# Optimization experiments

Hardware: AMD Instinct MI355X
Metric: run time of the kernel (lower is better)

## Reference

```python
import jax, jax.numpy as jnp
import numpy as np

NUM_CELLS = 2048
CELL_DIM = 256
N_STATES = 131072


def setup_inputs() -> dict:
    key = jax.random.key(0)
    k1, k2 = jax.random.split(key)
    x = jax.random.normal(k1, (N_STATES, CELL_DIM), dtype=jnp.float32)
    placeCells = jax.random.normal(k2, (NUM_CELLS, CELL_DIM), dtype=jnp.float32)
    return {"x": x, "placeCells": placeCells}


def reference(x, placeCells):
    # states: (N, cellDim); sims: (N, numCells); output: (N,) int argmax
    states = x.reshape(-1, CELL_DIM)
    sims = jnp.matmul(states, placeCells.T)  # (N, numCells) dense similarity
    return jnp.argmax(sims, axis=1)
```

## Files before the change

kernel.cpp:

```cpp
#include <hip/hip_runtime.h>
#include <float.h>
#include <stdint.h>

#define NUM_CELLS 2048
#define CELL_DIM  256
#define N_STATES  131072

typedef _Float16 half8 __attribute__((ext_vector_type(8)));
typedef float    f32x4 __attribute__((ext_vector_type(4)));

#define M1 0.10f
#define M2 0.004f
#define CAP1 32768
#define CAP2 4096

#define WS_C1 0
#define WS_C2 4
#define WS_L1 1024
#define WS_L2 (1024 + 4 * CAP1)
#define WS_PH 262144
#define WS_PL (262144 + 1048576)
#define WS_NEEDED (WS_PL + 1048576)

__device__ __forceinline__ void gld_lds16(const void* g, void* l) {
    __builtin_amdgcn_global_load_lds(
        (const __attribute__((address_space(1))) void*)g,
        (__attribute__((address_space(3))) void*)l, 16, 0, 0);
}

__global__ void prep_p(const float* __restrict__ p, _Float16* __restrict__ ph,
                       _Float16* __restrict__ pl, int* __restrict__ c1,
                       int* __restrict__ c2) {
    int d = blockIdx.x * 256 + threadIdx.x;
    if (d == 0) { *c1 = 0; *c2 = 0; }
    int l = d & 63, kf = (d >> 6) & 7, ct = d >> 9;
    int cell = ct * 16 + (l & 15);
    int k0 = kf * 32 + (l >> 4) * 8;
    const float* s = p + cell * 256 + k0;
    float4 a = *(const float4*)s, b = *(const float4*)(s + 4);
    float v[8] = {a.x, a.y, a.z, a.w, b.x, b.y, b.z, b.w};
    half8 h, lo;
#pragma unroll
    for (int j = 0; j < 8; ++j) {
        _Float16 hi = (_Float16)v[j];
        h[j] = hi;
        lo[j] = (_Float16)((v[j] - (float)hi) * 2048.0f);
    }
    *(half8*)(ph + (size_t)d * 8) = h;
    *(half8*)(pl + (size_t)d * 8) = lo;
}

__launch_bounds__(512, 2)
__global__ void pc_gemm1(const float* __restrict__ x, const _Float16* __restrict__ ph,
                         int* __restrict__ out, int* __restrict__ c1,
                         int* __restrict__ l1) {
    __shared__ _Float16 smem[32768];

    const int tid = threadIdx.x;
    const int l = tid & 63;
    const int w = tid >> 6;
    const int wr = w >> 2, wc = w & 3;

    const float* xg = x + (size_t)blockIdx.x * (128 * CELL_DIM);
#pragma unroll
    for (int i = 0; i < 8; ++i) {
        int d = tid + i * 512;
        int dl = d & 63, kf = (d >> 6) & 7, rt = d >> 9;
        int row = rt * 16 + (dl & 15);
        int k0 = kf * 32 + (dl >> 4) * 8;
        const float* s = xg + row * 256 + k0;
        float4 a = *(const float4*)s, b = *(const float4*)(s + 4);
        half8 h;
        h[0] = (_Float16)a.x; h[1] = (_Float16)a.y;
        h[2] = (_Float16)a.z; h[3] = (_Float16)a.w;
        h[4] = (_Float16)b.x; h[5] = (_Float16)b.y;
        h[6] = (_Float16)b.z; h[7] = (_Float16)b.w;
        *(half8*)(smem + d * 8) = h;
    }
    __syncthreads();

    half8 A[4][8];
#pragma unroll
    for (int rt = 0; rt < 4; ++rt)
#pragma unroll
        for (int kf = 0; kf < 8; ++kf)
            A[rt][kf] = *(const half8*)(smem + (((wr * 4 + rt) * 8 + kf) * 64 + l) * 8);
    __syncthreads();

    const char* pbase = (const char*)ph;
    auto stage = [&](int c) {
        char* dst = (char*)smem + (c & 1) * 32768;
        const char* src = pbase + (size_t)c * 32768;
#pragma unroll
        for (int i = 0; i < 4; ++i) {
            int off = w * 4096 + i * 1024;
            gld_lds16(src + off + l * 16, dst + off);
        }
    };

    float t1[16], t2[16];
    int ic[16];
#pragma unroll
    for (int s = 0; s < 16; ++s) { t1[s] = -FLT_MAX; t2[s] = -FLT_MAX; ic[s] = 0; }

    stage(0);
    __syncthreads();

    for (int c = 0; c < 32; ++c) {
        if (c < 31) stage(c + 1);
        const _Float16* pb = smem + (c & 1) * 16384 + wc * 4096;
        f32x4 a0 = {}, a1 = {}, a2 = {}, a3 = {};
#pragma unroll
        for (int kf = 0; kf < 8; ++kf) {
            half8 B = *(const half8*)(pb + kf * 512 + l * 8);
            a0 = __builtin_amdgcn_mfma_f32_16x16x32_f16(A[0][kf], B, a0, 0, 0, 0);
            a1 = __builtin_amdgcn_mfma_f32_16x16x32_f16(A[1][kf], B, a1, 0, 0, 0);
            a2 = __builtin_amdgcn_mfma_f32_16x16x32_f16(A[2][kf], B, a2, 0, 0, 0);
            a3 = __builtin_amdgcn_mfma_f32_16x16x32_f16(A[3][kf], B, a3, 0, 0, 0);
        }
#define UPD(ACC, RT)                                                       \
        _Pragma("unroll")                                                  \
        for (int reg = 0; reg < 4; ++reg) {                                \
            int s = (RT) * 4 + reg;                                        \
            float v = (ACC)[reg];                                          \
            float nt2 = __builtin_amdgcn_fmed3f(t1[s], t2[s], v);          \
            ic[s] = (v > t1[s]) ? c : ic[s];                               \
            t1[s] = fmaxf(t1[s], v);                                       \
            t2[s] = nt2;                                                   \
        }
        UPD(a0, 0) UPD(a1, 1) UPD(a2, 2) UPD(a3, 3)
#undef UPD
        __syncthreads();
    }

    int idx[16];
#pragma unroll
    for (int s = 0; s < 16; ++s) idx[s] = ic[s] * 64 + wc * 16 + (l & 15);
#pragma unroll
    for (int m = 1; m <= 8; m <<= 1) {
#pragma unroll
        for (int s = 0; s < 16; ++s) {
            float ot1 = __shfl_xor(t1[s], m, 64);
            int   oi  = __shfl_xor(idx[s], m, 64);
            float ot2 = __shfl_xor(t2[s], m, 64);
            float nt2 = fmaxf(fminf(t1[s], ot1), fmaxf(t2[s], ot2));
            if (ot1 > t1[s] || (ot1 == t1[s] && oi < idx[s])) { t1[s] = ot1; idx[s] = oi; }
            t2[s] = nt2;
        }
    }

    float* rT1 = (float*)smem;
    int*   rI1 = (int*)smem + 512;
    float* rT2 = (float*)smem + 1024;
    if ((l & 15) == 0) {
#pragma unroll
        for (int rt = 0; rt < 4; ++rt)
#pragma unroll
            for (int reg = 0; reg < 4; ++reg) {
                int s = rt * 4 + reg;
                int row = wr * 64 + rt * 16 + (l >> 4) * 4 + reg;
                rT1[row * 4 + wc] = t1[s];
                rI1[row * 4 + wc] = idx[s];
                rT2[row * 4 + wc] = t2[s];
            }
    }
    __syncthreads();
    if (tid < 128) {
        float T1 = -FLT_MAX, T2 = -FLT_MAX; int I1 = 0x7FFFFFFF;
#pragma unroll
        for (int g = 0; g < 4; ++g) {
            float v1 = rT1[tid * 4 + g];
            int   vi = rI1[tid * 4 + g];
            float v2 = rT2[tid * 4 + g];
            float nt2 = fmaxf(fminf(T1, v1), fmaxf(T2, v2));
            if (v1 > T1 || (v1 == T1 && vi < I1)) { T1 = v1; I1 = vi; }
            T2 = nt2;
        }
        int grow = blockIdx.x * 128 + tid;
        out[grow] = I1;
        if (T1 - T2 < M1) {
            int pos = atomicAdd(c1, 1);
            if (pos < CAP1) l1[pos] = grow;
        }
    }
}

__launch_bounds__(256, 2)
__global__ void pc_rescue2(const float* __restrict__ x, const _Float16* __restrict__ ph,
                           const _Float16* __restrict__ pl,
                           const int* __restrict__ c1, const int* __restrict__ l1,
                           int* __restrict__ out, int* __restrict__ c2,
                           int* __restrict__ l2) {
    __shared__ _Float16 sB[32768];
    const int n = *c1;
    const int base = blockIdx.x * 32;
    if (base >= n) return;
    const int tid = threadIdx.x;
    const int l = tid & 63, w = tid >> 6;
    const int wr = w >> 1, wc = w & 1;

    const int rslot = base + wr * 16 + (l & 15);
    const int my_row = l1[rslot < n ? rslot : (n - 1)];

    half8 Ah[8], Al[8];
#pragma unroll
    for (int kf = 0; kf < 8; ++kf) {
        const float* s = x + (size_t)my_row * 256 + kf * 32 + (l >> 4) * 8;
        float4 a = *(const float4*)s, b = *(const float4*)(s + 4);
        float v[8] = {a.x, a.y, a.z, a.w, b.x, b.y, b.z, b.w};
#pragma unroll
        for (int j = 0; j < 8; ++j) {
            _Float16 hi = (_Float16)v[j];
            Ah[kf][j] = hi;
            Al[kf][j] = (_Float16)((v[j] - (float)hi) * 2048.0f);
        }
    }

    auto stageB = [&](int c) {
        char* dst = (char*)sB + (c & 1) * 32768;
        const char* sh = (const char*)ph + (size_t)c * 16384;
        const char* sl = (const char*)pl + (size_t)c * 16384;
#pragma unroll
        for (int i = 0; i < 4; ++i) {
            int off = w * 4096 + i * 1024;
            gld_lds16(sh + off + l * 16, dst + off);
            gld_lds16(sl + off + l * 16, dst + 16384 + off);
        }
    };

    float t1[4], t2[4];
    int ic[4];
#pragma unroll
    for (int s = 0; s < 4; ++s) { t1[s] = -FLT_MAX; t2[s] = -FLT_MAX; ic[s] = 0; }

    stageB(0);
    __syncthreads();
    for (int c = 0; c < 64; ++c) {
        if (c < 63) stageB(c + 1);
        const _Float16* bh = sB + (c & 1) * 16384 + wc * 4096;
        const _Float16* bl = bh + 8192;
        f32x4 hh = {}, hl = {}, lh = {};
#pragma unroll
        for (int kf = 0; kf < 8; ++kf) {
            half8 Bh = *(const half8*)(bh + kf * 512 + l * 8);
            half8 Bl = *(const half8*)(bl + kf * 512 + l * 8);
            hh = __builtin_amdgcn_mfma_f32_16x16x32_f16(Ah[kf], Bh, hh, 0, 0, 0);
            hl = __builtin_amdgcn_mfma_f32_16x16x32_f16(Ah[kf], Bl, hl, 0, 0, 0);
            lh = __builtin_amdgcn_mfma_f32_16x16x32_f16(Al[kf], Bh, lh, 0, 0, 0);
        }
#pragma unroll
        for (int reg = 0; reg < 4; ++reg) {
            float v = hh[reg] + (hl[reg] + lh[reg]) * (1.0f / 2048.0f);
            float nt2 = __builtin_amdgcn_fmed3f(t1[reg], t2[reg], v);
            ic[reg] = (v > t1[reg]) ? c : ic[reg];
            t1[reg] = fmaxf(t1[reg], v);
            t2[reg] = nt2;
        }
        __syncthreads();
    }

    int idx[4];
#pragma unroll
    for (int s = 0; s < 4; ++s) idx[s] = ic[s] * 32 + wc * 16 + (l & 15);
#pragma unroll
    for (int m = 1; m <= 8; m <<= 1) {
#pragma unroll
        for (int s = 0; s < 4; ++s) {
            float ot1 = __shfl_xor(t1[s], m, 64);
            int   oi  = __shfl_xor(idx[s], m, 64);
            float ot2 = __shfl_xor(t2[s], m, 64);
            float nt2 = fmaxf(fminf(t1[s], ot1), fmaxf(t2[s], ot2));
            if (ot1 > t1[s] || (ot1 == t1[s] && oi < idx[s])) { t1[s] = ot1; idx[s] = oi; }
            t2[s] = nt2;
        }
    }

    float* rT1 = (float*)sB;
    int*   rI1 = (int*)sB + 64;
    float* rT2 = (float*)sB + 128;
    if ((l & 15) == 0) {
#pragma unroll
        for (int reg = 0; reg < 4; ++reg) {
            int row = wr * 16 + (l >> 4) * 4 + reg;
            rT1[row * 2 + wc] = t1[reg];
            rI1[row * 2 + wc] = idx[reg];
            rT2[row * 2 + wc] = t2[reg];
        }
    }
    __syncthreads();
    if (tid < 32) {
        float T1 = -FLT_MAX, T2 = -FLT_MAX; int I1 = 0x7FFFFFFF;
#pragma unroll
        for (int g = 0; g < 2; ++g) {
            float v1 = rT1[tid * 2 + g];
            int   vi = rI1[tid * 2 + g];
            float v2 = rT2[tid * 2 + g];
            float nt2 = fmaxf(fminf(T1, v1), fmaxf(T2, v2));
            if (v1 > T1 || (v1 == T1 && vi < I1)) { T1 = v1; I1 = vi; }
            T2 = nt2;
        }
        int slot = base + tid;
        if (slot < n) {
            int grow = l1[slot];
            out[grow] = I1;
            if (T1 - T2 < M2) {
                int pos = atomicAdd(c2, 1);
                if (pos < CAP2) l2[pos] = grow;
            }
        }
    }
}

__global__ void rescue3(const float* __restrict__ x, const float* __restrict__ p,
                        const int* __restrict__ count, const int* __restrict__ list,
                        int* __restrict__ out) {
    __shared__ float xrow[256];
    __shared__ float pch[32][260];
    __shared__ float red2[32][9];
    __shared__ float bvs[32];
    __shared__ int   bis[32];
    const int tid = threadIdx.x;
    const int n = *count;
    for (int e = blockIdx.x; e < n; e += gridDim.x) {
        const int row = list[e];
        __syncthreads();
        if (tid < 64) {
            float4 v = *(const float4*)(x + (size_t)row * 256 + tid * 4);
            *(float4*)(&xrow[tid * 4]) = v;
        }
        float bv = -FLT_MAX; int bi = 0;
        const int cell = tid & 31, kq = tid >> 5;
        for (int c0 = 0; c0 < NUM_CELLS; c0 += 32) {
            __syncthreads();
#pragma unroll
            for (int i = 0; i < 8; ++i) {
                int f = tid + i * 256;
                int cr = f >> 6, k4 = (f & 63) * 4;
                float4 v = *(const float4*)(p + (size_t)(c0 + cr) * 256 + k4);
                *(float4*)(&pch[cr][k4]) = v;
            }
            __syncthreads();
            float s = 0.f;
#pragma unroll
            for (int j = 0; j < 8; ++j) {
                float4 pv = *(const float4*)(&pch[cell][kq * 32 + j * 4]);
                float4 xv = *(const float4*)(&xrow[kq * 32 + j * 4]);
                s = fmaf(xv.x, pv.x, s); s = fmaf(xv.y, pv.y, s);
                s = fmaf(xv.z, pv.z, s); s = fmaf(xv.w, pv.w, s);
            }
            red2[cell][kq] = s;
            __syncthreads();
            if (tid < 32) {
                float dot = 0.f;
#pragma unroll
                for (int q = 0; q < 8; ++q) dot += red2[tid][q];
                if (dot > bv) { bv = dot; bi = c0 + tid; }
            }
        }
        if (tid < 32) { bvs[tid] = bv; bis[tid] = bi; }
        __syncthreads();
        if (tid == 0) {
            float B = bvs[0]; int BI = bis[0];
#pragma unroll
            for (int t = 1; t < 32; ++t)
                if (bvs[t] > B || (bvs[t] == B && bis[t] < BI)) { B = bvs[t]; BI = bis[t]; }
            out[row] = BI;
        }
    }
}

#define BM 64
#define BN 64
#define BK 32
#define XP 260
#define PP 68
__launch_bounds__(256, 2)
__global__ void placecells_argmax_fp32(const float* __restrict__ x,
                                       const float* __restrict__ pc,
                                       int* __restrict__ out) {
    __shared__ float xs[BM * XP];
    __shared__ float ps[BK * PP];
    const int tid = threadIdx.x;
    const int tx = tid & 15;
    const int ty = tid >> 4;
    const float* xg = x + (size_t)blockIdx.x * (BM * CELL_DIM);
#pragma unroll
    for (int i = 0; i < 16; ++i) {
        int f = tid + i * 256;
        int s = f >> 6, k4 = (f & 63) << 2;
        *(float4*)(&xs[s * XP + k4]) = *(const float4*)(xg + s * CELL_DIM + k4);
    }
    __syncthreads();
    float runv[4]; int runi[4];
#pragma unroll
    for (int si = 0; si < 4; ++si) { runv[si] = -FLT_MAX; runi[si] = 0; }
    for (int jc = 0; jc < NUM_CELLS; jc += BN) {
        float acc[4][4];
#pragma unroll
        for (int si = 0; si < 4; ++si)
#pragma unroll
            for (int cj = 0; cj < 4; ++cj) acc[si][cj] = 0.0f;
        for (int kc = 0; kc < CELL_DIM; kc += BK) {
            __syncthreads();
#pragma unroll
            for (int i = 0; i < 2; ++i) {
                int f = tid + i * 256;
                int c = f >> 3, k4 = (f & 7) << 2;
                float4 v = *(const float4*)(pc + (size_t)(jc + c) * CELL_DIM + kc + k4);
                ps[(k4 + 0) * PP + c] = v.x; ps[(k4 + 1) * PP + c] = v.y;
                ps[(k4 + 2) * PP + c] = v.z; ps[(k4 + 3) * PP + c] = v.w;
            }
            __syncthreads();
#pragma unroll
            for (int kk = 0; kk < BK; kk += 4) {
                float4 xv[4];
#pragma unroll
                for (int si = 0; si < 4; ++si)
                    xv[si] = *(const float4*)(&xs[(ty * 4 + si) * XP + kc + kk]);
#pragma unroll
                for (int kt = 0; kt < 4; ++kt) {
                    float4 pv = *(const float4*)(&ps[(kk + kt) * PP + tx * 4]);
#pragma unroll
                    for (int si = 0; si < 4; ++si) {
                        float xk = (kt == 0) ? xv[si].x : (kt == 1) ? xv[si].y :
                                   (kt == 2) ? xv[si].z : xv[si].w;
                        acc[si][0] = fmaf(xk, pv.x, acc[si][0]);
                        acc[si][1] = fmaf(xk, pv.y, acc[si][1]);
                        acc[si][2] = fmaf(xk, pv.z, acc[si][2]);
                        acc[si][3] = fmaf(xk, pv.w, acc[si][3]);
                    }
                }
            }
        }
#pragma unroll
        for (int si = 0; si < 4; ++si)
#pragma unroll
            for (int cj = 0; cj < 4; ++cj) {
                int idx = jc + tx * 4 + cj;
                if (acc[si][cj] > runv[si]) { runv[si] = acc[si][cj]; runi[si] = idx; }
            }
    }
    __syncthreads();
    float* rv = ps; int* ri = (int*)(ps + 1024);
#pragma unroll
    for (int si = 0; si < 4; ++si) {
        int s = ty * 4 + si;
        rv[s * 16 + tx] = runv[si]; ri[s * 16 + tx] = runi[si];
    }
    __syncthreads();
    if (tid < BM) {
        float bv = rv[tid * 16]; int bi = ri[tid * 16];
#pragma unroll
        for (int t = 1; t < 16; ++t) {
            float v = rv[tid * 16 + t]; int i = ri[tid * 16 + t];
            if (v > bv || (v == bv && i < bi)) { bv = v; bi = i; }
        }
        out[(size_t)blockIdx.x * BM + tid] = bi;
    }
}

extern "C" void kernel_launch(void* const* d_in, const int* in_sizes, int n_in,
                              void* d_out, int out_size, void* d_ws, size_t ws_size,
                              hipStream_t stream) {
    const float* x  = (const float*)d_in[0];
    const float* pc = (const float*)d_in[1];
    int* out = (int*)d_out;

    if (ws_size >= (size_t)WS_NEEDED) {
        char* ws = (char*)d_ws;
        int* c1 = (int*)(ws + WS_C1);
        int* c2 = (int*)(ws + WS_C2);
        int* l1 = (int*)(ws + WS_L1);
        int* l2 = (int*)(ws + WS_L2);
        _Float16* ph = (_Float16*)(ws + WS_PH);
        _Float16* pl = (_Float16*)(ws + WS_PL);
        prep_p<<<256, 256, 0, stream>>>(pc, ph, pl, c1, c2);
        pc_gemm1<<<N_STATES / 128, 512, 0, stream>>>(x, ph, out, c1, l1);
        pc_rescue2<<<CAP1 / 32, 256, 0, stream>>>(x, ph, pl, c1, l1, out, c2, l2);
        rescue3<<<64, 256, 0, stream>>>(x, pc, c2, l2, out);
    } else {
        placecells_argmax_fp32<<<N_STATES / BM, 256, 0, stream>>>(x, pc, out);
    }
}
```

Baseline: 505.1 us.

## Stream B fragments from global into registers, drop LDS staging and barriers

Both the main fp16 GEMM and the rescue kernel stop staging place-cell tiles through LDS with global_load_lds and per-tile barriers. Each wave now prefetches its B fragments straight from global memory (L2) into a rotating register buffer, and the column-to-cell index mapping changes to match. The rescue kernel also shrinks to 16 rows per block, which doubles its grid, and rescue3 gets a larger grid. The second-stage margin is tightened so fewer rows reach the exact fp32 fallback, and the list counts are now clamped to their caps. The tradeoff is more L2 traffic and more register pressure, plus a narrower margin that makes near-tie correctness more dependent on the fp16 hi/lo split being accurate.

```diff
diff --git a/kernel.cpp b/kernel.cpp
--- a/kernel.cpp
+++ b/kernel.cpp
@@ -10,23 +10,17 @@
 typedef float    f32x4 __attribute__((ext_vector_type(4)));
 
 #define M1 0.10f
-#define M2 0.004f
+#define M2 0.0008f
 #define CAP1 32768
 #define CAP2 4096
 
 #define WS_C1 0
 #define WS_C2 4
 #define WS_L1 1024
-#define WS_L2 (1024 + 4 * CAP1)
+#define WS_L2 (WS_L1 + 4 * CAP1)
 #define WS_PH 262144
-#define WS_PL (262144 + 1048576)
-#define WS_NEEDED (WS_PL + 1048576)
-
-__device__ __forceinline__ void gld_lds16(const void* g, void* l) {
-    __builtin_amdgcn_global_load_lds(
-        (const __attribute__((address_space(1))) void*)g,
-        (__attribute__((address_space(3))) void*)l, 16, 0, 0);
-}
+#define WS_PL (WS_PH + 1048576)
+#define WS_NEEDED (WS_PL + 1048576 + 131072)
 
 __global__ void prep_p(const float* __restrict__ p, _Float16* __restrict__ ph,
                        _Float16* __restrict__ pl, int* __restrict__ c1,
@@ -87,36 +81,31 @@
             A[rt][kf] = *(const half8*)(smem + (((wr * 4 + rt) * 8 + kf) * 64 + l) * 8);
     __syncthreads();
 
-    const char* pbase = (const char*)ph;
-    auto stage = [&](int c) {
-        char* dst = (char*)smem + (c & 1) * 32768;
-        const char* src = pbase + (size_t)c * 32768;
-#pragma unroll
-        for (int i = 0; i < 4; ++i) {
-            int off = w * 4096 + i * 1024;
-            gld_lds16(src + off + l * 16, dst + off);
-        }
-    };
+    const _Float16* bb = ph + wc * 4096 + (size_t)l * 8;
+
+    half8 Bf[4];
+    Bf[0] = *(const half8*)(bb + 0);
+    Bf[1] = *(const half8*)(bb + 512);
+    Bf[2] = *(const half8*)(bb + 1024);
+    Bf[3] = *(const half8*)(bb + 1536);
 
     float t1[16], t2[16];
     int ic[16];
 #pragma unroll
     for (int s = 0; s < 16; ++s) { t1[s] = -FLT_MAX; t2[s] = -FLT_MAX; ic[s] = 0; }
 
-    stage(0);
-    __syncthreads();
-
-    for (int c = 0; c < 32; ++c) {
-        if (c < 31) stage(c + 1);
-        const _Float16* pb = smem + (c & 1) * 16384 + wc * 4096;
+    for (int t = 0; t < 32; ++t) {
+        const _Float16* bt = bb + t * 16384;
         f32x4 a0 = {}, a1 = {}, a2 = {}, a3 = {};
 #pragma unroll
-        for (int kf = 0; kf < 8; ++kf) {
-            half8 B = *(const half8*)(pb + kf * 512 + l * 8);
-            a0 = __builtin_amdgcn_mfma_f32_16x16x32_f16(A[0][kf], B, a0, 0, 0, 0);
-            a1 = __builtin_amdgcn_mfma_f32_16x16x32_f16(A[1][kf], B, a1, 0, 0, 0);
-            a2 = __builtin_amdgcn_mfma_f32_16x16x32_f16(A[2][kf], B, a2, 0, 0, 0);
-            a3 = __builtin_amdgcn_mfma_f32_16x16x32_f16(A[3][kf], B, a3, 0, 0, 0);
+        for (int k = 0; k < 8; ++k) {
+            half8 B = Bf[k & 3];
+            Bf[k & 3] = *(const half8*)(bt + ((k < 4) ? (k + 4) * 512
+                                                      : (16384 + (k - 4) * 512)));
+            a0 = __builtin_amdgcn_mfma_f32_16x16x32_f16(A[0][k], B, a0, 0, 0, 0);
+            a1 = __builtin_amdgcn_mfma_f32_16x16x32_f16(A[1][k], B, a1, 0, 0, 0);
+            a2 = __builtin_amdgcn_mfma_f32_16x16x32_f16(A[2][k], B, a2, 0, 0, 0);
+            a3 = __builtin_amdgcn_mfma_f32_16x16x32_f16(A[3][k], B, a3, 0, 0, 0);
         }
 #define UPD(ACC, RT)                                                       \
         _Pragma("unroll")                                                  \
@@ -124,18 +113,17 @@
             int s = (RT) * 4 + reg;                                        \
             float v = (ACC)[reg];                                          \
             float nt2 = __builtin_amdgcn_fmed3f(t1[s], t2[s], v);          \
-            ic[s] = (v > t1[s]) ? c : ic[s];                               \
+            ic[s] = (v > t1[s]) ? t : ic[s];                               \
             t1[s] = fmaxf(t1[s], v);                                       \
             t2[s] = nt2;                                                   \
         }
         UPD(a0, 0) UPD(a1, 1) UPD(a2, 2) UPD(a3, 3)
 #undef UPD
-        __syncthreads();
     }
 
     int idx[16];
 #pragma unroll
-    for (int s = 0; s < 16; ++s) idx[s] = ic[s] * 64 + wc * 16 + (l & 15);
+    for (int s = 0; s < 16; ++s) idx[s] = (ic[s] * 4 + wc) * 16 + (l & 15);
 #pragma unroll
     for (int m = 1; m <= 8; m <<= 1) {
 #pragma unroll
@@ -191,15 +179,14 @@
                            const int* __restrict__ c1, const int* __restrict__ l1,
                            int* __restrict__ out, int* __restrict__ c2,
                            int* __restrict__ l2) {
-    __shared__ _Float16 sB[32768];
-    const int n = *c1;
-    const int base = blockIdx.x * 32;
+    const int n0 = *c1;
+    const int n = n0 < CAP1 ? n0 : CAP1;
+    const int base = blockIdx.x * 16;
     if (base >= n) return;
     const int tid = threadIdx.x;
-    const int l = tid & 63, w = tid >> 6;
-    const int wr = w >> 1, wc = w & 1;
-
-    const int rslot = base + wr * 16 + (l & 15);
+    const int l = tid & 63, wc = tid >> 6;
+
+    const int rslot = base + (l & 15);
     const int my_row = l1[rslot < n ? rslot : (n - 1)];
 
     half8 Ah[8], Al[8];
@@ -216,52 +203,47 @@
         }
     }
 
-    auto stageB = [&](int c) {
-        char* dst = (char*)sB + (c & 1) * 32768;
-        const char* sh = (const char*)ph + (size_t)c * 16384;
-        const char* sl = (const char*)pl + (size_t)c * 16384;
-#pragma unroll
-        for (int i = 0; i < 4; ++i) {
-            int off = w * 4096 + i * 1024;
-            gld_lds16(sh + off + l * 16, dst + off);
-            gld_lds16(sl + off + l * 16, dst + 16384 + off);
-        }
-    };
+    const _Float16* bh = ph + wc * 4096 + (size_t)l * 8;
+    const _Float16* bl = pl + wc * 4096 + (size_t)l * 8;
+    half8 BH[4], BL[4];
+#pragma unroll
+    for (int j = 0; j < 4; ++j) {
+        BH[j] = *(const half8*)(bh + j * 512);
+        BL[j] = *(const half8*)(bl + j * 512);
+    }
 
     float t1[4], t2[4];
     int ic[4];
 #pragma unroll
     for (int s = 0; s < 4; ++s) { t1[s] = -FLT_MAX; t2[s] = -FLT_MAX; ic[s] = 0; }
 
-    stageB(0);
-    __syncthreads();
-    for (int c = 0; c < 64; ++c) {
-        if (c < 63) stageB(c + 1);
-        const _Float16* bh = sB + (c & 1) * 16384 + wc * 4096;
-        const _Float16* bl = bh + 8192;
+    for (int t = 0; t < 32; ++t) {
+        const _Float16* bth = bh + t * 16384;
+        const _Float16* btl = bl + t * 16384;
         f32x4 hh = {}, hl = {}, lh = {};
 #pragma unroll
-        for (int kf = 0; kf < 8; ++kf) {
-            half8 Bh = *(const half8*)(bh + kf * 512 + l * 8);
-            half8 Bl = *(const half8*)(bl + kf * 512 + l * 8);
-            hh = __builtin_amdgcn_mfma_f32_16x16x32_f16(Ah[kf], Bh, hh, 0, 0, 0);
-            hl = __builtin_amdgcn_mfma_f32_16x16x32_f16(Ah[kf], Bl, hl, 0, 0, 0);
-            lh = __builtin_amdgcn_mfma_f32_16x16x32_f16(Al[kf], Bh, lh, 0, 0, 0);
+        for (int k = 0; k < 8; ++k) {
+            half8 Bh_ = BH[k & 3], Bl_ = BL[k & 3];
+            int off = (k < 4) ? (k + 4) * 512 : (16384 + (k - 4) * 512);
+            BH[k & 3] = *(const half8*)(bth + off);
+            BL[k & 3] = *(const half8*)(btl + off);
+            hh = __builtin_amdgcn_mfma_f32_16x16x32_f16(Ah[k], Bh_, hh, 0, 0, 0);
+            hl = __builtin_amdgcn_mfma_f32_16x16x32_f16(Ah[k], Bl_, hl, 0, 0, 0);
+            lh = __builtin_amdgcn_mfma_f32_16x16x32_f16(Al[k], Bh_, lh, 0, 0, 0);
         }
 #pragma unroll
         for (int reg = 0; reg < 4; ++reg) {
             float v = hh[reg] + (hl[reg] + lh[reg]) * (1.0f / 2048.0f);
             float nt2 = __builtin_amdgcn_fmed3f(t1[reg], t2[reg], v);
-            ic[reg] = (v > t1[reg]) ? c : ic[reg];
+            ic[reg] = (v > t1[reg]) ? t : ic[reg];
             t1[reg] = fmaxf(t1[reg], v);
             t2[reg] = nt2;
         }
-        __syncthreads();
     }
 
     int idx[4];
 #pragma unroll
-    for (int s = 0; s < 4; ++s) idx[s] = ic[s] * 32 + wc * 16 + (l & 15);
+    for (int s = 0; s < 4; ++s) idx[s] = (ic[s] * 4 + wc) * 16 + (l & 15);
 #pragma unroll
     for (int m = 1; m <= 8; m <<= 1) {
 #pragma unroll
@@ -275,26 +257,26 @@
         }
     }
 
-    float* rT1 = (float*)sB;
-    int*   rI1 = (int*)sB + 64;
-    float* rT2 = (float*)sB + 128;
+    __shared__ float rT1[64];
+    __shared__ int   rI1[64];
+    __shared__ float rT2[64];
     if ((l & 15) == 0) {
 #pragma unroll
         for (int reg = 0; reg < 4; ++reg) {
-            int row = wr * 16 + (l >> 4) * 4 + reg;
-            rT1[row * 2 + wc] = t1[reg];
-            rI1[row * 2 + wc] = idx[reg];
-            rT2[row * 2 + wc] = t2[reg];
-        }
-    }
-    __syncthreads();
-    if (tid < 32) {
+            int r = (l >> 4) * 4 + reg;
+            rT1[r * 4 + wc] = t1[reg];
+            rI1[r * 4 + wc] = idx[reg];
+            rT2[r * 4 + wc] = t2[reg];
+        }
+    }
+    __syncthreads();
+    if (tid < 16) {
         float T1 = -FLT_MAX, T2 = -FLT_MAX; int I1 = 0x7FFFFFFF;
 #pragma unroll
-        for (int g = 0; g < 2; ++g) {
-            float v1 = rT1[tid * 2 + g];
-            int   vi = rI1[tid * 2 + g];
-            float v2 = rT2[tid * 2 + g];
+        for (int g = 0; g < 4; ++g) {
+            float v1 = rT1[tid * 4 + g];
+            int   vi = rI1[tid * 4 + g];
+            float v2 = rT2[tid * 4 + g];
             float nt2 = fmaxf(fminf(T1, v1), fmaxf(T2, v2));
             if (v1 > T1 || (v1 == T1 && vi < I1)) { T1 = v1; I1 = vi; }
             T2 = nt2;
@@ -320,7 +302,8 @@
     __shared__ float bvs[32];
     __shared__ int   bis[32];
     const int tid = threadIdx.x;
-    const int n = *count;
+    const int n0 = *count;
+    const int n = n0 < CAP2 ? n0 : CAP2;
     for (int e = blockIdx.x; e < n; e += gridDim.x) {
         const int row = list[e];
         __syncthreads();
@@ -476,8 +459,8 @@
         _Float16* pl = (_Float16*)(ws + WS_PL);
         prep_p<<<256, 256, 0, stream>>>(pc, ph, pl, c1, c2);
         pc_gemm1<<<N_STATES / 128, 512, 0, stream>>>(x, ph, out, c1, l1);
-        pc_rescue2<<<CAP1 / 32, 256, 0, stream>>>(x, ph, pl, c1, l1, out, c2, l2);
-        rescue3<<<64, 256, 0, stream>>>(x, pc, c2, l2, out);
+        pc_rescue2<<<CAP1 / 16, 256, 0, stream>>>(x, ph, pl, c1, l1, out, c2, l2);
+        rescue3<<<128, 256, 0, stream>>>(x, pc, c2, l2, out);
     } else {
         placecells_argmax_fp32<<<N_STATES / BM, 256, 0, stream>>>(x, pc, out);
     }
```

Measured after the change: 514.7 us. About the same (+1.9%).
